# Performance work log

Measured on AMD Instinct MI355X. Metric: run time of the kernel, lower is better.

The kernel has to match this reference:

```python
import jax, jax.numpy as jnp
import numpy as np

ITERATIONS = 3  # init_kwargs: adjacency power order

def setup_inputs() -> dict:
    key = jax.random.key(0)
    ks = jax.random.split(key, 8)
    n_nodes = 100000
    in_ch, out_ch = 512, 128
    nnz_feat = 1600000
    n_edges = 1600000
    feat_rows = jax.random.randint(ks[0], (nnz_feat,), 0, n_nodes, dtype=jnp.int32)
    feat_cols = jax.random.randint(ks[1], (nnz_feat,), 0, in_ch, dtype=jnp.int32)
    feat_values = jax.random.uniform(ks[2], (nnz_feat,), dtype=jnp.float32)
    adj_rows = jax.random.randint(ks[3], (n_edges,), 0, n_nodes, dtype=jnp.int32)
    adj_cols = jax.random.randint(ks[4], (n_edges,), 0, n_nodes, dtype=jnp.int32)
    # normalized adjacency values (positive, roughly 1/degree scale)
    adj_values = jax.random.uniform(ks[5], (n_edges,), dtype=jnp.float32) / 16.0
    # xavier-uniform-like init
    bound_w = float(np.sqrt(6.0 / (in_ch + out_ch)))
    weight = jax.random.uniform(ks[6], (in_ch, out_ch), minval=-bound_w, maxval=bound_w, dtype=jnp.float32)
    bound_b = float(np.sqrt(6.0 / (1 + out_ch)))
    bias = jax.random.uniform(ks[7], (1, out_ch), minval=-bound_b, maxval=bound_b, dtype=jnp.float32)
    return {"feat_rows": feat_rows, "feat_cols": feat_cols, "feat_values": feat_values,
            "adj_rows": adj_rows, "adj_cols": adj_cols, "adj_values": adj_values,
            "weight": weight, "bias": bias, "n_nodes": n_nodes}

def reference(feat_rows, feat_cols, feat_values, adj_rows, adj_cols, adj_values, weight, bias, n_nodes):
    # SpMM: (sparse features [n_nodes, in_ch]) @ weight [in_ch, out_ch]
    # base[r] = sum over nnz with row r of val * weight[col]
    contrib = feat_values[:, None] * weight[feat_cols]           # [nnz, out_ch]
    base = jax.ops.segment_sum(contrib, feat_rows, num_segments=n_nodes)  # [n_nodes, out_ch]
    # bias + dropout (eval mode: identity) + relu
    base = jax.nn.relu(base + bias)
    # iterative sparse propagation: base = A_norm @ base, (iterations - 1) times
    for _ in range(ITERATIONS - 1):
        msgs = adj_values[:, None] * base[adj_cols]              # [n_edges, out_ch]
        base = jax.ops.segment_sum(msgs, adj_rows, num_segments=n_nodes)
    return base
```

## Files before the change

kernel.cpp:

```cpp
#include <hip/hip_runtime.h>
#include <hip/hip_fp16.h>


#define CH 128
#define BR 128
#define SCAN_BLK 1024
#define BIN_WGS 256
#define BIN_THR 512


__global__ void bucket_hist_kernel(const int* __restrict__ rows, int* __restrict__ wg_counts,
                                   int nE, int nbuck, int chunk) {
    extern __shared__ int hcnt[];
    const int tid = threadIdx.x;
    const long long T = blockDim.x;
    long long start = (long long)blockIdx.x * chunk;
    long long end = start + chunk;
    if (end > nE) end = nE;
    for (int b = tid; b < nbuck; b += blockDim.x) hcnt[b] = 0;
    __syncthreads();
    if (start < end) {
        long long i = start + tid;
        for (; i + 3 * T < end; i += 4 * T) {
            int r0 = rows[i], r1 = rows[i + T], r2 = rows[i + 2 * T], r3 = rows[i + 3 * T];
            atomicAdd(&hcnt[r0 >> 7], 1);
            atomicAdd(&hcnt[r1 >> 7], 1);
            atomicAdd(&hcnt[r2 >> 7], 1);
            atomicAdd(&hcnt[r3 >> 7], 1);
        }
        for (; i < end; i += T) atomicAdd(&hcnt[rows[i] >> 7], 1);
    }
    __syncthreads();
    for (int b = tid; b < nbuck; b += blockDim.x)
        wg_counts[(long long)blockIdx.x * nbuck + b] = hcnt[b];
}

__global__ void wgscan_kernel(int* __restrict__ wg_counts, int* __restrict__ bcounts,
                              int nbuck, int nwg) {
    int b = blockIdx.x * (blockDim.x >> 6) + (threadIdx.x >> 6);
    int lane = threadIdx.x & 63;
    if (b >= nbuck) return;
    int carry = 0;
    for (int base = 0; base < nwg; base += 64) {
        int wg = base + lane;
        int v = (wg < nwg) ? wg_counts[(long long)wg * nbuck + b] : 0;
        int x = v;
        #pragma unroll
        for (int off = 1; off < 64; off <<= 1) {
            int y = __shfl_up(x, off);
            if (lane >= off) x += y;
        }
        if (wg < nwg) wg_counts[(long long)wg * nbuck + b] = carry + x - v;
        carry += __shfl(x, 63);
    }
    if (lane == 0) bcounts[b] = carry;
}

__global__ void bucket_scan_kernel(const int* __restrict__ bcounts,
                                   int* __restrict__ bucket_base, int* __restrict__ row_ptr_n,
                                   int nbuck) {
    __shared__ int lds[SCAN_BLK];
    int tid = threadIdx.x;
    int x = (tid < nbuck) ? bcounts[tid] : 0;
    lds[tid] = x;
    __syncthreads();
    for (int off = 1; off < SCAN_BLK; off <<= 1) {
        int y = (tid >= off) ? lds[tid - off] : 0;
        __syncthreads();
        lds[tid] += y;
        __syncthreads();
    }
    if (tid < nbuck) bucket_base[tid] = lds[tid] - x;
    if (tid == nbuck - 1) {
        bucket_base[nbuck] = lds[tid];
        *row_ptr_n = lds[tid];
    }
}

__global__ void multisplit_bin_kernel(const int* __restrict__ rows, const int* __restrict__ cols,
                                      const float* __restrict__ vals,
                                      const int* __restrict__ bbase,
                                      const int* __restrict__ wg_counts,
                                      int2* __restrict__ cv_tmp, int nE, int nbuck, int chunk) {
    extern __shared__ int lds[];
    int* hcnt  = lds;
    int* hbase = lds + nbuck;
    const int tid = threadIdx.x;
    const long long T = blockDim.x;
    long long start = (long long)blockIdx.x * chunk;
    long long end = start + chunk;
    if (end > nE) end = nE;
    for (int b = tid; b < nbuck; b += blockDim.x) {
        hbase[b] = bbase[b] + wg_counts[(long long)blockIdx.x * nbuck + b];
        hcnt[b] = 0;
    }
    __syncthreads();
    if (start >= end) return;
    long long i = start + tid;
    for (; i + 3 * T < end; i += 4 * T) {
        int r0 = rows[i], r1 = rows[i + T], r2 = rows[i + 2 * T], r3 = rows[i + 3 * T];
        int c0 = cols[i], c1 = cols[i + T], c2 = cols[i + 2 * T], c3 = cols[i + 3 * T];
        float v0 = vals[i], v1 = vals[i + T], v2 = vals[i + 2 * T], v3 = vals[i + 3 * T];
        int b0 = r0 >> 7, b1 = r1 >> 7, b2 = r2 >> 7, b3 = r3 >> 7;
        int p0 = hbase[b0] + atomicAdd(&hcnt[b0], 1);
        int p1 = hbase[b1] + atomicAdd(&hcnt[b1], 1);
        int p2 = hbase[b2] + atomicAdd(&hcnt[b2], 1);
        int p3 = hbase[b3] + atomicAdd(&hcnt[b3], 1);
        cv_tmp[p0] = make_int2(c0 | ((r0 & (BR - 1)) << 24), __float_as_int(v0));
        cv_tmp[p1] = make_int2(c1 | ((r1 & (BR - 1)) << 24), __float_as_int(v1));
        cv_tmp[p2] = make_int2(c2 | ((r2 & (BR - 1)) << 24), __float_as_int(v2));
        cv_tmp[p3] = make_int2(c3 | ((r3 & (BR - 1)) << 24), __float_as_int(v3));
    }
    for (; i < end; i += T) {
        int r = rows[i];
        int b = r >> 7;
        int p = hbase[b] + atomicAdd(&hcnt[b], 1);
        cv_tmp[p] = make_int2(cols[i] | ((r & (BR - 1)) << 24), __float_as_int(vals[i]));
    }
}

__global__ void reorder2_kernel(const int* __restrict__ bucket_base,
                                const int2* __restrict__ cv_tmp, int2* __restrict__ cv,
                                int* __restrict__ row_ptr, int n) {
    __shared__ int cnt[BR];
    __shared__ int tmp[BR];
    int b = blockIdx.x;
    int rbase = b * BR;
    int tid = threadIdx.x;
    int s = bucket_base[b], e = bucket_base[b + 1];
    if (tid < BR) cnt[tid] = 0;
    __syncthreads();
    for (int i = s + tid; i < e; i += blockDim.x)
        atomicAdd(&cnt[((unsigned)cv_tmp[i].x) >> 24], 1);
    __syncthreads();
    if (tid < BR) tmp[tid] = cnt[tid];
    __syncthreads();
    for (int off = 1; off < BR; off <<= 1) {
        int y = 0;
        if (tid < BR && tid >= off) y = tmp[tid - off];
        __syncthreads();
        if (tid < BR) tmp[tid] += y;
        __syncthreads();
    }
    if (tid < BR) {
        int excl = s + tmp[tid] - cnt[tid];
        if (rbase + tid < n) row_ptr[rbase + tid] = excl;
        cnt[tid] = excl;
    }
    __syncthreads();
    for (int i = s + tid; i < e; i += blockDim.x) {
        int2 ent = cv_tmp[i];
        int rl = ((unsigned)ent.x) >> 24;
        int p = atomicAdd(&cnt[rl], 1);
        cv[p] = make_int2(ent.x & 0x00FFFFFF, ent.y);
    }
}


__global__ void wconv_kernel(const float* __restrict__ W, __half2* __restrict__ Wh, int n2) {
    int i = blockIdx.x * blockDim.x + threadIdx.x;
    if (i < n2) Wh[i] = __float22half2_rn(reinterpret_cast<const float2*>(W)[i]);
}


__global__ void spmm_g4_kernel(const int* __restrict__ row_ptr,
                               const long long* __restrict__ cv,
                               const __half2* __restrict__ Wh,
                               const float* __restrict__ bias,
                               __half2* __restrict__ outh, int n) {
    __shared__ long long sc[4 * 64];
    int gtid = blockIdx.x * blockDim.x + threadIdx.x;
    int wid = gtid >> 6;
    int lane = gtid & 63;
    if (wid >= n) return;
    int g = lane >> 4;
    int cl = lane & 15;
    long long* mysc = sc + (threadIdx.x >> 6) * 64;
    int s = row_ptr[wid], e = row_ptr[wid + 1];
    float acc0 = 0.f, acc1 = 0.f, acc2 = 0.f, acc3 = 0.f;
    float acc4 = 0.f, acc5 = 0.f, acc6 = 0.f, acc7 = 0.f;
    for (int base = s; base < e; base += 64) {
        int idx = base + lane;
        mysc[lane] = (idx < e) ? cv[idx] : 0;
        int m = e - base; if (m > 64) m = 64;
        for (int k0 = 0; k0 < m; k0 += 4) {
            long long ck = mysc[k0 + g];
            int col = (int)ck;
            float v = __int_as_float((int)(ck >> 32));
            float4 wv = *reinterpret_cast<const float4*>(Wh + (long long)col * 64 + cl * 4);
            float2 f0 = __half22float2(*reinterpret_cast<const __half2*>(&wv.x));
            float2 f1 = __half22float2(*reinterpret_cast<const __half2*>(&wv.y));
            float2 f2 = __half22float2(*reinterpret_cast<const __half2*>(&wv.z));
            float2 f3 = __half22float2(*reinterpret_cast<const __half2*>(&wv.w));
            acc0 += v * f0.x; acc1 += v * f0.y;
            acc2 += v * f1.x; acc3 += v * f1.y;
            acc4 += v * f2.x; acc5 += v * f2.y;
            acc6 += v * f3.x; acc7 += v * f3.y;
        }
    }
    acc0 += __shfl_xor(acc0, 16); acc1 += __shfl_xor(acc1, 16);
    acc2 += __shfl_xor(acc2, 16); acc3 += __shfl_xor(acc3, 16);
    acc4 += __shfl_xor(acc4, 16); acc5 += __shfl_xor(acc5, 16);
    acc6 += __shfl_xor(acc6, 16); acc7 += __shfl_xor(acc7, 16);
    acc0 += __shfl_xor(acc0, 32); acc1 += __shfl_xor(acc1, 32);
    acc2 += __shfl_xor(acc2, 32); acc3 += __shfl_xor(acc3, 32);
    acc4 += __shfl_xor(acc4, 32); acc5 += __shfl_xor(acc5, 32);
    acc6 += __shfl_xor(acc6, 32); acc7 += __shfl_xor(acc7, 32);
    if (g == 0) {
        const float4* bp = reinterpret_cast<const float4*>(bias);
        float4 b0 = bp[cl * 2], b1 = bp[cl * 2 + 1];
        acc0 = fmaxf(acc0 + b0.x, 0.f); acc1 = fmaxf(acc1 + b0.y, 0.f);
        acc2 = fmaxf(acc2 + b0.z, 0.f); acc3 = fmaxf(acc3 + b0.w, 0.f);
        acc4 = fmaxf(acc4 + b1.x, 0.f); acc5 = fmaxf(acc5 + b1.y, 0.f);
        acc6 = fmaxf(acc6 + b1.z, 0.f); acc7 = fmaxf(acc7 + b1.w, 0.f);
        __half2 h0 = __floats2half2_rn(acc0, acc1);
        __half2 h1 = __floats2half2_rn(acc2, acc3);
        __half2 h2 = __floats2half2_rn(acc4, acc5);
        __half2 h3 = __floats2half2_rn(acc6, acc7);
        float4 ov;
        *reinterpret_cast<__half2*>(&ov.x) = h0;
        *reinterpret_cast<__half2*>(&ov.y) = h1;
        *reinterpret_cast<__half2*>(&ov.z) = h2;
        *reinterpret_cast<__half2*>(&ov.w) = h3;
        *reinterpret_cast<float4*>(outh + (long long)wid * 64 + cl * 4) = ov;
    }
}

__global__ void prop_g4_h2h_kernel(const int* __restrict__ row_ptr,
                                   const long long* __restrict__ cv,
                                   const __half2* __restrict__ src, __half2* __restrict__ dst,
                                   int n) {
    __shared__ long long sc[4 * 64];
    int gtid = blockIdx.x * blockDim.x + threadIdx.x;
    int wid = gtid >> 6;
    int lane = gtid & 63;
    if (wid >= n) return;
    int g = lane >> 4;
    int cl = lane & 15;
    long long* mysc = sc + (threadIdx.x >> 6) * 64;
    int s = row_ptr[wid], e = row_ptr[wid + 1];
    float acc0 = 0.f, acc1 = 0.f, acc2 = 0.f, acc3 = 0.f;
    float acc4 = 0.f, acc5 = 0.f, acc6 = 0.f, acc7 = 0.f;
    for (int base = s; base < e; base += 64) {
        int idx = base + lane;
        mysc[lane] = (idx < e) ? cv[idx] : 0;
        int m = e - base; if (m > 64) m = 64;
        for (int k0 = 0; k0 < m; k0 += 4) {
            long long ck = mysc[k0 + g];
            int col = (int)ck;
            float v = __int_as_float((int)(ck >> 32));
            float4 sv = *reinterpret_cast<const float4*>(src + (long long)col * 64 + cl * 4);
            float2 f0 = __half22float2(*reinterpret_cast<const __half2*>(&sv.x));
            float2 f1 = __half22float2(*reinterpret_cast<const __half2*>(&sv.y));
            float2 f2 = __half22float2(*reinterpret_cast<const __half2*>(&sv.z));
            float2 f3 = __half22float2(*reinterpret_cast<const __half2*>(&sv.w));
            acc0 += v * f0.x; acc1 += v * f0.y;
            acc2 += v * f1.x; acc3 += v * f1.y;
            acc4 += v * f2.x; acc5 += v * f2.y;
            acc6 += v * f3.x; acc7 += v * f3.y;
        }
    }
    acc0 += __shfl_xor(acc0, 16); acc1 += __shfl_xor(acc1, 16);
    acc2 += __shfl_xor(acc2, 16); acc3 += __shfl_xor(acc3, 16);
    acc4 += __shfl_xor(acc4, 16); acc5 += __shfl_xor(acc5, 16);
    acc6 += __shfl_xor(acc6, 16); acc7 += __shfl_xor(acc7, 16);
    acc0 += __shfl_xor(acc0, 32); acc1 += __shfl_xor(acc1, 32);
    acc2 += __shfl_xor(acc2, 32); acc3 += __shfl_xor(acc3, 32);
    acc4 += __shfl_xor(acc4, 32); acc5 += __shfl_xor(acc5, 32);
    acc6 += __shfl_xor(acc6, 32); acc7 += __shfl_xor(acc7, 32);
    if (g == 0) {
        __half2 h0 = __floats2half2_rn(acc0, acc1);
        __half2 h1 = __floats2half2_rn(acc2, acc3);
        __half2 h2 = __floats2half2_rn(acc4, acc5);
        __half2 h3 = __floats2half2_rn(acc6, acc7);
        float4 ov;
        *reinterpret_cast<__half2*>(&ov.x) = h0;
        *reinterpret_cast<__half2*>(&ov.y) = h1;
        *reinterpret_cast<__half2*>(&ov.z) = h2;
        *reinterpret_cast<__half2*>(&ov.w) = h3;
        *reinterpret_cast<float4*>(dst + (long long)wid * 64 + cl * 4) = ov;
    }
}

__global__ void prop_g4_h2f_kernel(const int* __restrict__ row_ptr,
                                   const long long* __restrict__ cv,
                                   const __half2* __restrict__ src, float* __restrict__ dst,
                                   int n) {
    __shared__ long long sc[4 * 64];
    int gtid = blockIdx.x * blockDim.x + threadIdx.x;
    int wid = gtid >> 6;
    int lane = gtid & 63;
    if (wid >= n) return;
    int g = lane >> 4;
    int cl = lane & 15;
    long long* mysc = sc + (threadIdx.x >> 6) * 64;
    int s = row_ptr[wid], e = row_ptr[wid + 1];
    float acc0 = 0.f, acc1 = 0.f, acc2 = 0.f, acc3 = 0.f;
    float acc4 = 0.f, acc5 = 0.f, acc6 = 0.f, acc7 = 0.f;
    for (int base = s; base < e; base += 64) {
        int idx = base + lane;
        mysc[lane] = (idx < e) ? cv[idx] : 0;
        int m = e - base; if (m > 64) m = 64;
        for (int k0 = 0; k0 < m; k0 += 4) {
            long long ck = mysc[k0 + g];
            int col = (int)ck;
            float v = __int_as_float((int)(ck >> 32));
            float4 sv = *reinterpret_cast<const float4*>(src + (long long)col * 64 + cl * 4);
            float2 f0 = __half22float2(*reinterpret_cast<const __half2*>(&sv.x));
            float2 f1 = __half22float2(*reinterpret_cast<const __half2*>(&sv.y));
            float2 f2 = __half22float2(*reinterpret_cast<const __half2*>(&sv.z));
            float2 f3 = __half22float2(*reinterpret_cast<const __half2*>(&sv.w));
            acc0 += v * f0.x; acc1 += v * f0.y;
            acc2 += v * f1.x; acc3 += v * f1.y;
            acc4 += v * f2.x; acc5 += v * f2.y;
            acc6 += v * f3.x; acc7 += v * f3.y;
        }
    }
    acc0 += __shfl_xor(acc0, 16); acc1 += __shfl_xor(acc1, 16);
    acc2 += __shfl_xor(acc2, 16); acc3 += __shfl_xor(acc3, 16);
    acc4 += __shfl_xor(acc4, 16); acc5 += __shfl_xor(acc5, 16);
    acc6 += __shfl_xor(acc6, 16); acc7 += __shfl_xor(acc7, 16);
    acc0 += __shfl_xor(acc0, 32); acc1 += __shfl_xor(acc1, 32);
    acc2 += __shfl_xor(acc2, 32); acc3 += __shfl_xor(acc3, 32);
    acc4 += __shfl_xor(acc4, 32); acc5 += __shfl_xor(acc5, 32);
    acc6 += __shfl_xor(acc6, 32); acc7 += __shfl_xor(acc7, 32);
    if (g == 0) {
        float4 o0 = make_float4(acc0, acc1, acc2, acc3);
        float4 o1 = make_float4(acc4, acc5, acc6, acc7);
        float4* dp = reinterpret_cast<float4*>(dst + (long long)wid * 128 + cl * 8);
        dp[0] = o0;
        dp[1] = o1;
    }
}


__global__ void bias_relu_kernel(float* __restrict__ buf, const float* __restrict__ bias,
                                 long long total) {
    long long i = ((long long)blockIdx.x * blockDim.x + threadIdx.x) * 4;
    if (i >= total) return;
    float4 v = *reinterpret_cast<float4*>(buf + i);
    int ch = (int)(i & (CH - 1));
    float4 b = *reinterpret_cast<const float4*>(bias + ch);
    v.x = fmaxf(v.x + b.x, 0.0f);
    v.y = fmaxf(v.y + b.y, 0.0f);
    v.z = fmaxf(v.z + b.z, 0.0f);
    v.w = fmaxf(v.w + b.w, 0.0f);
    *reinterpret_cast<float4*>(buf + i) = v;
}

__global__ void spmm_scatter_kernel(const int* __restrict__ rows, const int* __restrict__ cols,
                                    const float* __restrict__ vals, const float* __restrict__ weight,
                                    float* __restrict__ out, int nnz) {
    long long tid = (long long)blockIdx.x * blockDim.x + threadIdx.x;
    if (tid >= (long long)nnz * 32) return;
    int e = (int)(tid >> 5), lane = (int)(tid & 31);
    int r = rows[e], c = cols[e];
    float v = vals[e];
    const float4 w = *reinterpret_cast<const float4*>(weight + (long long)c * CH + lane * 4);
    float* dst = out + (long long)r * CH + lane * 4;
    unsafeAtomicAdd(dst + 0, v * w.x);
    unsafeAtomicAdd(dst + 1, v * w.y);
    unsafeAtomicAdd(dst + 2, v * w.z);
    unsafeAtomicAdd(dst + 3, v * w.w);
}

__global__ void prop_scatter_kernel(const int* __restrict__ rows, const int* __restrict__ cols,
                                    const float* __restrict__ vals, const float* __restrict__ src,
                                    float* __restrict__ dst, int ne) {
    long long tid = (long long)blockIdx.x * blockDim.x + threadIdx.x;
    if (tid >= (long long)ne * 32) return;
    int e = (int)(tid >> 5), lane = (int)(tid & 31);
    int r = rows[e], c = cols[e];
    float v = vals[e];
    const float4 s = *reinterpret_cast<const float4*>(src + (long long)c * CH + lane * 4);
    float* d = dst + (long long)r * CH + lane * 4;
    unsafeAtomicAdd(d + 0, v * s.x);
    unsafeAtomicAdd(d + 1, v * s.y);
    unsafeAtomicAdd(d + 2, v * s.z);
    unsafeAtomicAdd(d + 3, v * s.w);
}


static inline size_t align64(size_t x) { return (x + 63) & ~(size_t)63; }

extern "C" void kernel_launch(void* const* d_in, const int* in_sizes, int n_in,
                              void* d_out, int out_size, void* d_ws, size_t ws_size,
                              hipStream_t stream) {
    const int*   feat_rows = (const int*)d_in[0];
    const int*   feat_cols = (const int*)d_in[1];
    const float* feat_vals = (const float*)d_in[2];
    const int*   adj_rows  = (const int*)d_in[3];
    const int*   adj_cols  = (const int*)d_in[4];
    const float* adj_vals  = (const float*)d_in[5];
    const float* weight    = (const float*)d_in[6];
    const float* bias      = (const float*)d_in[7];

    const int nnz = in_sizes[0];
    const int ne  = in_sizes[3];
    const int n   = out_size / CH;
    const int in_ch = in_sizes[6] / CH;

    float* out = (float*)d_out;
    char*  ws  = (char*)d_ws;

    const size_t NBF = (size_t)n * CH * sizeof(float);
    const size_t NBH = (size_t)n * CH * sizeof(__half);
    const long long total_elems = (long long)n * CH;
    const int BLK = 256;
    const int ew_blocks = (int)((total_elems / 4 + BLK - 1) / BLK);
    const int maxe = nnz > ne ? nnz : ne;
    const int nbuck = (n + BR - 1) / BR;
    const size_t bin_lds = (size_t)nbuck * 2 * sizeof(int);

    size_t off = 0;
    __half2* baseh    = (__half2*)(ws + off); off += align64(NBH);
    __half2* pingh    = (__half2*)(ws + off); off += align64(NBH);
    int*   row_ptr   = (int*)(ws + off);   off += align64(((size_t)n + 1) * 4);
    int*   bcounts   = (int*)(ws + off);   off += align64((size_t)nbuck * 4);
    int*   bbase     = (int*)(ws + off);   off += align64(((size_t)nbuck + 1) * 4);
    int*   wg_counts = (int*)(ws + off);   off += align64((size_t)BIN_WGS * nbuck * 4);
    __half2* Wh      = (__half2*)(ws + off); off += align64((size_t)in_ch * 64 * 4);
    int2*  cv        = (int2*)(ws + off);  off += align64((size_t)maxe * 8);
    int2*  cv_tmp    = (int2*)pingh;
    const bool fast = (ws_size >= off) && (nbuck <= SCAN_BLK) &&
                      (n <= (1 << 24)) && (bin_lds <= 64 * 1024) &&
                      (in_ch <= (1 << 22)) &&
                      ((size_t)maxe * 8 <= NBH);

    if (fast) {
        const int row_blocks = (int)(((long long)n * 64 + BLK - 1) / BLK);
        const int chunk_feat = (nnz + BIN_WGS - 1) / BIN_WGS;
        const int chunk_adj  = (ne + BIN_WGS - 1) / BIN_WGS;
        const int w2 = in_ch * 64;
        const size_t hist_lds = (size_t)nbuck * sizeof(int);
        const int wgscan_blocks = (nbuck + 3) / 4;

        wconv_kernel<<<(w2 + BLK - 1) / BLK, BLK, 0, stream>>>(weight, Wh, w2);

        bucket_hist_kernel<<<BIN_WGS, BIN_THR, hist_lds, stream>>>(
            feat_rows, wg_counts, nnz, nbuck, chunk_feat);
        wgscan_kernel<<<wgscan_blocks, 256, 0, stream>>>(wg_counts, bcounts, nbuck, BIN_WGS);
        bucket_scan_kernel<<<1, SCAN_BLK, 0, stream>>>(bcounts, bbase, row_ptr + n, nbuck);
        multisplit_bin_kernel<<<BIN_WGS, BIN_THR, bin_lds, stream>>>(
            feat_rows, feat_cols, feat_vals, bbase, wg_counts, cv_tmp, nnz, nbuck, chunk_feat);
        reorder2_kernel<<<nbuck, BIN_THR, 0, stream>>>(bbase, cv_tmp, cv, row_ptr, n);
        spmm_g4_kernel<<<row_blocks, BLK, 0, stream>>>(
            row_ptr, (const long long*)cv, Wh, bias, baseh, n);

        bucket_hist_kernel<<<BIN_WGS, BIN_THR, hist_lds, stream>>>(
            adj_rows, wg_counts, ne, nbuck, chunk_adj);
        wgscan_kernel<<<wgscan_blocks, 256, 0, stream>>>(wg_counts, bcounts, nbuck, BIN_WGS);
        bucket_scan_kernel<<<1, SCAN_BLK, 0, stream>>>(bcounts, bbase, row_ptr + n, nbuck);
        multisplit_bin_kernel<<<BIN_WGS, BIN_THR, bin_lds, stream>>>(
            adj_rows, adj_cols, adj_vals, bbase, wg_counts, cv_tmp, ne, nbuck, chunk_adj);
        reorder2_kernel<<<nbuck, BIN_THR, 0, stream>>>(bbase, cv_tmp, cv, row_ptr, n);
        prop_g4_h2h_kernel<<<row_blocks, BLK, 0, stream>>>(
            row_ptr, (const long long*)cv, baseh, pingh, n);
        prop_g4_h2f_kernel<<<row_blocks, BLK, 0, stream>>>(
            row_ptr, (const long long*)cv, pingh, out, n);
    } else {
        float* ping = (float*)ws;
        const int spmm_blocks = (int)(((long long)nnz * 32 + BLK - 1) / BLK);
        const int prop_blocks = (int)(((long long)ne * 32 + BLK - 1) / BLK);
        hipMemsetAsync(d_out, 0, NBF, stream);
        spmm_scatter_kernel<<<spmm_blocks, BLK, 0, stream>>>(feat_rows, feat_cols, feat_vals,
                                                             weight, out, nnz);
        bias_relu_kernel<<<ew_blocks, BLK, 0, stream>>>(out, bias, total_elems);
        hipMemsetAsync(ping, 0, NBF, stream);
        prop_scatter_kernel<<<prop_blocks, BLK, 0, stream>>>(adj_rows, adj_cols, adj_vals,
                                                             out, ping, ne);
        hipMemsetAsync(d_out, 0, NBF, stream);
        prop_scatter_kernel<<<prop_blocks, BLK, 0, stream>>>(adj_rows, adj_cols, adj_vals,
                                                             ping, out, ne);
    }
}
```

Baseline: 253.2 us.

## Batch feature and adjacency binning passes into shared histogram, scan and bin kernels

The histogram, per-workgroup scan, bucket scan and multisplit binning for the feature matrix and the adjacency matrix now run together in single launches. Block index selects the matrix, so each kernel gets twice as many workgroups and there are fewer launches and serial gaps. Both staging buffers live side by side in the ping buffer, which tightens the fast-path size condition. The row_ptr[n] write moves into the reorder kernel. An unroll-4 pragma is also added to the gather loops of the SpMM and propagation kernels.

```diff
diff --git a/kernel.cpp b/kernel.cpp
--- a/kernel.cpp
+++ b/kernel.cpp
@@ -9,12 +9,18 @@
 #define BIN_THR 512
 
 
-__global__ void bucket_hist_kernel(const int* __restrict__ rows, int* __restrict__ wg_counts,
-                                   int nE, int nbuck, int chunk) {
+__global__ void hist2_kernel(const int* __restrict__ rows_f, int nf, int chunk_f,
+                             const int* __restrict__ rows_a, int na, int chunk_a,
+                             int* __restrict__ wgc, int nbuck) {
     extern __shared__ int hcnt[];
+    const int m  = blockIdx.x >> 8;
+    const int wg = blockIdx.x & (BIN_WGS - 1);
+    const int* rows = m ? rows_a : rows_f;
+    const int nE    = m ? na : nf;
+    const int chunk = m ? chunk_a : chunk_f;
     const int tid = threadIdx.x;
     const long long T = blockDim.x;
-    long long start = (long long)blockIdx.x * chunk;
+    long long start = (long long)wg * chunk;
     long long end = start + chunk;
     if (end > nE) end = nE;
     for (int b = tid; b < nbuck; b += blockDim.x) hcnt[b] = 0;
@@ -31,37 +37,41 @@
         for (; i < end; i += T) atomicAdd(&hcnt[rows[i] >> 7], 1);
     }
     __syncthreads();
-    for (int b = tid; b < nbuck; b += blockDim.x)
-        wg_counts[(long long)blockIdx.x * nbuck + b] = hcnt[b];
-}
-
-__global__ void wgscan_kernel(int* __restrict__ wg_counts, int* __restrict__ bcounts,
-                              int nbuck, int nwg) {
-    int b = blockIdx.x * (blockDim.x >> 6) + (threadIdx.x >> 6);
+    int* out = wgc + ((long long)m * BIN_WGS + wg) * nbuck;
+    for (int b = tid; b < nbuck; b += blockDim.x) out[b] = hcnt[b];
+}
+
+__global__ void wgscan2_kernel(int* __restrict__ wgc, int* __restrict__ bcounts,
+                               int nbuck, int nwg) {
+    int wpb = blockDim.x >> 6;
+    int idx = blockIdx.x * wpb + (threadIdx.x >> 6);
     int lane = threadIdx.x & 63;
-    if (b >= nbuck) return;
+    if (idx >= 2 * nbuck) return;
+    int m = (idx >= nbuck) ? 1 : 0;
+    int b = idx - m * nbuck;
+    int* base = wgc + (long long)m * nwg * nbuck + b;
     int carry = 0;
-    for (int base = 0; base < nwg; base += 64) {
-        int wg = base + lane;
-        int v = (wg < nwg) ? wg_counts[(long long)wg * nbuck + b] : 0;
+    for (int w0 = 0; w0 < nwg; w0 += 64) {
+        int wg = w0 + lane;
+        int v = (wg < nwg) ? base[(long long)wg * nbuck] : 0;
         int x = v;
         #pragma unroll
         for (int off = 1; off < 64; off <<= 1) {
             int y = __shfl_up(x, off);
             if (lane >= off) x += y;
         }
-        if (wg < nwg) wg_counts[(long long)wg * nbuck + b] = carry + x - v;
+        if (wg < nwg) base[(long long)wg * nbuck] = carry + x - v;
         carry += __shfl(x, 63);
     }
-    if (lane == 0) bcounts[b] = carry;
-}
-
-__global__ void bucket_scan_kernel(const int* __restrict__ bcounts,
-                                   int* __restrict__ bucket_base, int* __restrict__ row_ptr_n,
-                                   int nbuck) {
+    if (lane == 0) bcounts[idx] = carry;
+}
+
+__global__ void bucket_scan2_kernel(const int* __restrict__ bcounts,
+                                    int* __restrict__ bbase, int nbuck) {
     __shared__ int lds[SCAN_BLK];
+    int m = blockIdx.x;
     int tid = threadIdx.x;
-    int x = (tid < nbuck) ? bcounts[tid] : 0;
+    int x = (tid < nbuck) ? bcounts[m * nbuck + tid] : 0;
     lds[tid] = x;
     __syncthreads();
     for (int off = 1; off < SCAN_BLK; off <<= 1) {
@@ -70,28 +80,37 @@
         lds[tid] += y;
         __syncthreads();
     }
-    if (tid < nbuck) bucket_base[tid] = lds[tid] - x;
-    if (tid == nbuck - 1) {
-        bucket_base[nbuck] = lds[tid];
-        *row_ptr_n = lds[tid];
-    }
-}
-
-__global__ void multisplit_bin_kernel(const int* __restrict__ rows, const int* __restrict__ cols,
-                                      const float* __restrict__ vals,
-                                      const int* __restrict__ bbase,
-                                      const int* __restrict__ wg_counts,
-                                      int2* __restrict__ cv_tmp, int nE, int nbuck, int chunk) {
+    int* bb = bbase + m * (nbuck + 1);
+    if (tid < nbuck) bb[tid] = lds[tid] - x;
+    if (tid == nbuck - 1) bb[nbuck] = lds[tid];
+}
+
+__global__ void bin2_kernel(const int* __restrict__ rows_f, const int* __restrict__ cols_f,
+                            const float* __restrict__ vals_f, int nf, int chunk_f,
+                            const int* __restrict__ rows_a, const int* __restrict__ cols_a,
+                            const float* __restrict__ vals_a, int na, int chunk_a,
+                            const int* __restrict__ bbase, const int* __restrict__ wgc,
+                            int2* __restrict__ cvt_f, int2* __restrict__ cvt_a, int nbuck) {
     extern __shared__ int lds[];
     int* hcnt  = lds;
     int* hbase = lds + nbuck;
+    const int m  = blockIdx.x >> 8;
+    const int wg = blockIdx.x & (BIN_WGS - 1);
+    const int* rows = m ? rows_a : rows_f;
+    const int* cols = m ? cols_a : cols_f;
+    const float* vals = m ? vals_a : vals_f;
+    const int nE    = m ? na : nf;
+    const int chunk = m ? chunk_a : chunk_f;
+    int2* cv_tmp = m ? cvt_a : cvt_f;
+    const int* bb = bbase + m * (nbuck + 1);
+    const int* wc = wgc + ((long long)m * BIN_WGS + wg) * nbuck;
     const int tid = threadIdx.x;
     const long long T = blockDim.x;
-    long long start = (long long)blockIdx.x * chunk;
+    long long start = (long long)wg * chunk;
     long long end = start + chunk;
     if (end > nE) end = nE;
     for (int b = tid; b < nbuck; b += blockDim.x) {
-        hbase[b] = bbase[b] + wg_counts[(long long)blockIdx.x * nbuck + b];
+        hbase[b] = bb[b] + wc[b];
         hcnt[b] = 0;
     }
     __syncthreads();
@@ -147,6 +166,7 @@
         if (rbase + tid < n) row_ptr[rbase + tid] = excl;
         cnt[tid] = excl;
     }
+    if (tid == 0 && b == gridDim.x - 1) row_ptr[n] = e;
     __syncthreads();
     for (int i = s + tid; i < e; i += blockDim.x) {
         int2 ent = cv_tmp[i];
@@ -183,6 +203,7 @@
         int idx = base + lane;
         mysc[lane] = (idx < e) ? cv[idx] : 0;
         int m = e - base; if (m > 64) m = 64;
+        #pragma unroll 4
         for (int k0 = 0; k0 < m; k0 += 4) {
             long long ck = mysc[k0 + g];
             int col = (int)ck;
@@ -245,6 +266,7 @@
         int idx = base + lane;
         mysc[lane] = (idx < e) ? cv[idx] : 0;
         int m = e - base; if (m > 64) m = 64;
+        #pragma unroll 4
         for (int k0 = 0; k0 < m; k0 += 4) {
             long long ck = mysc[k0 + g];
             int col = (int)ck;
@@ -301,6 +323,7 @@
         int idx = base + lane;
         mysc[lane] = (idx < e) ? cv[idx] : 0;
         int m = e - base; if (m > 64) m = 64;
+        #pragma unroll 4
         for (int k0 = 0; k0 < m; k0 += 4) {
             long long ck = mysc[k0 + g];
             int col = (int)ck;
@@ -413,19 +436,20 @@
     const size_t bin_lds = (size_t)nbuck * 2 * sizeof(int);
 
     size_t off = 0;
-    __half2* baseh    = (__half2*)(ws + off); off += align64(NBH);
-    __half2* pingh    = (__half2*)(ws + off); off += align64(NBH);
-    int*   row_ptr   = (int*)(ws + off);   off += align64(((size_t)n + 1) * 4);
-    int*   bcounts   = (int*)(ws + off);   off += align64((size_t)nbuck * 4);
-    int*   bbase     = (int*)(ws + off);   off += align64(((size_t)nbuck + 1) * 4);
-    int*   wg_counts = (int*)(ws + off);   off += align64((size_t)BIN_WGS * nbuck * 4);
-    __half2* Wh      = (__half2*)(ws + off); off += align64((size_t)in_ch * 64 * 4);
-    int2*  cv        = (int2*)(ws + off);  off += align64((size_t)maxe * 8);
-    int2*  cv_tmp    = (int2*)pingh;
+    __half2* baseh   = (__half2*)(ws + off); off += align64(NBH);
+    __half2* pingh   = (__half2*)(ws + off); off += align64(NBH);
+    int*   row_ptr  = (int*)(ws + off);   off += align64(((size_t)n + 1) * 4);
+    int*   bcounts  = (int*)(ws + off);   off += align64((size_t)2 * nbuck * 4);
+    int*   bbase    = (int*)(ws + off);   off += align64((size_t)2 * (nbuck + 1) * 4);
+    int*   wgc      = (int*)(ws + off);   off += align64((size_t)2 * BIN_WGS * nbuck * 4);
+    __half2* Wh     = (__half2*)(ws + off); off += align64((size_t)in_ch * 64 * 4);
+    int2*  cv       = (int2*)(ws + off);  off += align64((size_t)maxe * 8);
+    int2*  cvt_f    = (int2*)pingh;
+    int2*  cvt_a    = (int2*)((char*)pingh + (size_t)nnz * 8);
     const bool fast = (ws_size >= off) && (nbuck <= SCAN_BLK) &&
                       (n <= (1 << 24)) && (bin_lds <= 64 * 1024) &&
                       (in_ch <= (1 << 22)) &&
-                      ((size_t)maxe * 8 <= NBH);
+                      (((size_t)nnz + (size_t)ne) * 8 <= NBH);
 
     if (fast) {
         const int row_blocks = (int)(((long long)n * 64 + BLK - 1) / BLK);
@@ -433,27 +457,24 @@
         const int chunk_adj  = (ne + BIN_WGS - 1) / BIN_WGS;
         const int w2 = in_ch * 64;
         const size_t hist_lds = (size_t)nbuck * sizeof(int);
-        const int wgscan_blocks = (nbuck + 3) / 4;
+        const int wgscan_blocks = (2 * nbuck + 3) / 4;
 
         wconv_kernel<<<(w2 + BLK - 1) / BLK, BLK, 0, stream>>>(weight, Wh, w2);
 
-        bucket_hist_kernel<<<BIN_WGS, BIN_THR, hist_lds, stream>>>(
-            feat_rows, wg_counts, nnz, nbuck, chunk_feat);
-        wgscan_kernel<<<wgscan_blocks, 256, 0, stream>>>(wg_counts, bcounts, nbuck, BIN_WGS);
-        bucket_scan_kernel<<<1, SCAN_BLK, 0, stream>>>(bcounts, bbase, row_ptr + n, nbuck);
-        multisplit_bin_kernel<<<BIN_WGS, BIN_THR, bin_lds, stream>>>(
-            feat_rows, feat_cols, feat_vals, bbase, wg_counts, cv_tmp, nnz, nbuck, chunk_feat);
-        reorder2_kernel<<<nbuck, BIN_THR, 0, stream>>>(bbase, cv_tmp, cv, row_ptr, n);
+        hist2_kernel<<<2 * BIN_WGS, BIN_THR, hist_lds, stream>>>(
+            feat_rows, nnz, chunk_feat, adj_rows, ne, chunk_adj, wgc, nbuck);
+        wgscan2_kernel<<<wgscan_blocks, 256, 0, stream>>>(wgc, bcounts, nbuck, BIN_WGS);
+        bucket_scan2_kernel<<<2, SCAN_BLK, 0, stream>>>(bcounts, bbase, nbuck);
+        bin2_kernel<<<2 * BIN_WGS, BIN_THR, bin_lds, stream>>>(
+            feat_rows, feat_cols, feat_vals, nnz, chunk_feat,
+            adj_rows, adj_cols, adj_vals, ne, chunk_adj,
+            bbase, wgc, cvt_f, cvt_a, nbuck);
+
+        reorder2_kernel<<<nbuck, BIN_THR, 0, stream>>>(bbase, cvt_f, cv, row_ptr, n);
         spmm_g4_kernel<<<row_blocks, BLK, 0, stream>>>(
             row_ptr, (const long long*)cv, Wh, bias, baseh, n);
 
-        bucket_hist_kernel<<<BIN_WGS, BIN_THR, hist_lds, stream>>>(
-            adj_rows, wg_counts, ne, nbuck, chunk_adj);
-        wgscan_kernel<<<wgscan_blocks, 256, 0, stream>>>(wg_counts, bcounts, nbuck, BIN_WGS);
-        bucket_scan_kernel<<<1, SCAN_BLK, 0, stream>>>(bcounts, bbase, row_ptr + n, nbuck);
-        multisplit_bin_kernel<<<BIN_WGS, BIN_THR, bin_lds, stream>>>(
-            adj_rows, adj_cols, adj_vals, bbase, wg_counts, cv_tmp, ne, nbuck, chunk_adj);
-        reorder2_kernel<<<nbuck, BIN_THR, 0, stream>>>(bbase, cv_tmp, cv, row_ptr, n);
+        reorder2_kernel<<<nbuck, BIN_THR, 0, stream>>>(bbase + (nbuck + 1), cvt_a, cv, row_ptr, n);
         prop_g4_h2h_kernel<<<row_blocks, BLK, 0, stream>>>(
             row_ptr, (const long long*)cv, baseh, pingh, n);
         prop_g4_h2f_kernel<<<row_blocks, BLK, 0, stream>>>(
```

Measured after the change: 246.1 us. 1.03x faster.
